# Kernel optimization log

Measured on AMD Instinct MI355X. Metric: run time of the kernel, lower is better.

The kernel has to match this reference:

```python
import jax, jax.numpy as jnp
import numpy as np

C = 512
C8 = C // 8  # 64
B, H, W = 4, 64, 64


def setup_inputs() -> dict:
    key = jax.random.key(0)
    ks = jax.random.split(key, 8)
    s_in = 1.0 / np.sqrt(C)
    return {
        "x": jax.random.normal(ks[0], (B, C, H, W), dtype=jnp.float32),
        "Wf": jax.random.normal(ks[1], (C8, C), dtype=jnp.float32) * s_in,
        "bf": jax.random.normal(ks[2], (C8,), dtype=jnp.float32) * 0.01,
        "Wg": jax.random.normal(ks[3], (C8, C), dtype=jnp.float32) * s_in,
        "bg": jax.random.normal(ks[4], (C8,), dtype=jnp.float32) * 0.01,
        "Wh": jax.random.normal(ks[5], (C, C), dtype=jnp.float32) * s_in,
        "bh": jax.random.normal(ks[6], (C,), dtype=jnp.float32) * 0.01,
        # original inits gamma=0; use small nonzero so the attention path is exercised
        "gamma": jax.random.normal(ks[7], (1,), dtype=jnp.float32) * 0.1,
    }


def reference(x, Wf, bf, Wg, bg, Wh, bh, gamma):
    b, c, h, w = x.shape
    n = h * w
    xt = x.reshape(b, c, n)  # flatten spatial -> tokens (b, C, N)
    # 1x1 convs are per-token GEMMs
    f = jnp.einsum('bcn,oc->bno', xt, Wf) + bf          # (b, N, C8)
    g = jnp.einsum('bcn,oc->bon', xt, Wg) + bg[:, None]  # (b, C8, N)
    attn = jax.nn.softmax(jnp.einsum('bnk,bkm->bnm', f, g), axis=2)  # (b, N, N)
    hv = jnp.einsum('bcn,oc->bon', xt, Wh) + bh[:, None]  # (b, C, N)
    # torch.bmm(h, attention): out[:,c,j] = sum_i h[:,c,i] * attn[:,i,j]
    sa = jnp.einsum('bci,bij->bcj', hv, attn).reshape(b, c, h, w)
    return gamma[0] * sa + x
```

## Files before the change

### kernel.cpp

```cpp
#include <hip/hip_runtime.h>


#define Bq 4
#define Cq 512
#define Nq 4096
#define PSTR 72

typedef __attribute__((ext_vector_type(8))) short bf16x8;
typedef __attribute__((ext_vector_type(4))) float f32x4;

__device__ __forceinline__ short f2bf(float f) {
  unsigned u = __float_as_uint(f);
  u += 0x7fffu + ((u >> 16) & 1u);
  return (short)(u >> 16);
}
__device__ __forceinline__ float bf2f(short h) {
  return __uint_as_float(((unsigned)(unsigned short)h) << 16);
}

#define MFMA16(A, B, C) __builtin_amdgcn_mfma_f32_16x16x32_bf16((A), (B), (C), 0, 0, 0)

__device__ __forceinline__ size_t fg_frag(int b, int t16, int ss) {
  return ((size_t)((b * 256 + t16) * 2 + ss)) * 512;
}
__device__ __forceinline__ size_t hv_frag(int b, int tc, int si) {
  return ((size_t)((b * 32 + tc) * 128 + si)) * 512;
}

__global__ __launch_bounds__(256) void k_prepw(
    const float* __restrict__ Wf, const float* __restrict__ Wg,
    const float* __restrict__ Wh,
    short* __restrict__ whi, short* __restrict__ wlo, short* __restrict__ whb) {
  int gid = blockIdx.x * 256 + threadIdx.x;
  if (gid < 128 * 512) {
    int row = gid >> 9;
    float v = (row < 64) ? Wf[gid] : Wg[gid - 32768];
    short h = f2bf(v);
    whi[gid] = h;
    wlo[gid] = f2bf(v - bf2f(h));
  }
  whb[gid] = f2bf(Wh[gid]);
}

__global__ __launch_bounds__(256) void k_xpose(
    const float* __restrict__ x, short* __restrict__ xthi, short* __restrict__ xtlo) {
  int b = blockIdx.z, c0 = blockIdx.y * 64, n0 = blockIdx.x * 64;
  __shared__ float tile[64][65];
  int t = threadIdx.x;
  int l = t & 15, g = t >> 4;
  const float* xp = x + ((size_t)b * Cq + c0) * Nq + n0;
#pragma unroll
  for (int e = 0; e < 4; e++) {
    int cl = g + e * 16;
    float4 v = *(const float4*)(xp + (size_t)cl * Nq + l * 4);
    tile[cl][l * 4 + 0] = v.x; tile[cl][l * 4 + 1] = v.y;
    tile[cl][l * 4 + 2] = v.z; tile[cl][l * 4 + 3] = v.w;
  }
  __syncthreads();
#pragma unroll
  for (int e = 0; e < 4; e++) {
    int nl = g + e * 16;
    short hi[4], lo[4];
#pragma unroll
    for (int qq = 0; qq < 4; qq++) {
      float v = tile[l * 4 + qq][nl];
      hi[qq] = f2bf(v);
      lo[qq] = f2bf(v - bf2f(hi[qq]));
    }
    size_t off = ((size_t)b * Nq + n0 + nl) * Cq + c0 + l * 4;
    *(short4*)(xthi + off) = make_short4(hi[0], hi[1], hi[2], hi[3]);
    *(short4*)(xtlo + off) = make_short4(lo[0], lo[1], lo[2], lo[3]);
  }
}

__global__ __launch_bounds__(512) void k_fg(
    const short* __restrict__ xthi, const short* __restrict__ xtlo,
    const short* __restrict__ whi, const short* __restrict__ wlo,
    const float* __restrict__ bfv, const float* __restrict__ bgv,
    short* __restrict__ ffh, short* __restrict__ ffl,
    short* __restrict__ gfh, short* __restrict__ gfl) {
  int b = blockIdx.y, n0 = blockIdx.x * 64;
  int t = threadIdx.x, w = t >> 6, lane = t & 63, l15 = lane & 15, q = lane >> 4;
  int wr = w & 3, wh = w >> 2;
  const short* ah = xthi + ((size_t)b * Nq + n0 + wr * 16 + l15) * Cq;
  const short* al = xtlo + ((size_t)b * Nq + n0 + wr * 16 + l15) * Cq;
  f32x4 z = {0.f, 0.f, 0.f, 0.f};
  f32x4 acc[4] = {z, z, z, z};
  for (int ks = 0; ks < 16; ks++) {
    bf16x8 Ahi = *(const bf16x8*)(ah + ks * 32 + q * 8);
    bf16x8 Alo = *(const bf16x8*)(al + ks * 32 + q * 8);
#pragma unroll
    for (int os = 0; os < 4; os++) {
      int o = wh * 64 + os * 16 + l15;
      bf16x8 Bhi = *(const bf16x8*)(whi + o * 512 + ks * 32 + q * 8);
      bf16x8 Blo = *(const bf16x8*)(wlo + o * 512 + ks * 32 + q * 8);
      acc[os] = MFMA16(Alo, Bhi, acc[os]);
      acc[os] = MFMA16(Ahi, Blo, acc[os]);
      acc[os] = MFMA16(Ahi, Bhi, acc[os]);
    }
  }
#pragma unroll
  for (int os = 0; os < 4; os++) {
#pragma unroll
    for (int r = 0; r < 4; r++) {
      int o = os * 16 + l15;
      int n = n0 + wr * 16 + q * 4 + r;
      float v = acc[os][r] + (wh == 0 ? bfv[o] : bgv[o]);
      size_t off = ((size_t)((b * 256 + (n >> 4)) * 2 + (o >> 5))) * 512
                 + (((o >> 3) & 3) * 16 + (n & 15)) * 8 + (o & 7);
      short h = f2bf(v);
      short lo = f2bf(v - bf2f(h));
      if (wh == 0) { ffh[off] = h; ffl[off] = lo; }
      else         { gfh[off] = h; gfl[off] = lo; }
    }
  }
}

__global__ __launch_bounds__(512) void k_stats(
    const short* __restrict__ ffh, const short* __restrict__ ffl,
    const short* __restrict__ gfh, const short* __restrict__ gfl,
    float* __restrict__ lsum4) {
  int jch = blockIdx.x, jc = jch * 1024, i0 = blockIdx.y * 64, b = blockIdx.z;
  int t = threadIdx.x, w = t >> 6, lane = t & 63, l15 = lane & 15, q = lane >> 4;
  bf16x8 Ahi[4][2], Alo[4][2];
#pragma unroll
  for (int ig = 0; ig < 4; ig++)
#pragma unroll
    for (int ss = 0; ss < 2; ss++) {
      size_t base = fg_frag(b, (i0 >> 4) + ig, ss) + lane * 8;
      Ahi[ig][ss] = *(const bf16x8*)(ffh + base);
      Alo[ig][ss] = *(const bf16x8*)(ffl + base);
    }
  float ls[16];
#pragma unroll
  for (int a = 0; a < 16; a++) ls[a] = 0.f;
  f32x4 z = {0.f, 0.f, 0.f, 0.f};
  for (int jt = 0; jt < 8; jt++) {
    int tj = (jc >> 4) + w * 8 + jt;
    bf16x8 GBh[2], GBl[2];
#pragma unroll
    for (int ss = 0; ss < 2; ss++) {
      size_t base = fg_frag(b, tj, ss) + lane * 8;
      GBh[ss] = *(const bf16x8*)(gfh + base);
      GBl[ss] = *(const bf16x8*)(gfl + base);
    }
#pragma unroll
    for (int ig = 0; ig < 4; ig++) {
      f32x4 sh = z, sl = z;
#pragma unroll
      for (int ss = 0; ss < 2; ss++) {
        sl = MFMA16(Alo[ig][ss], GBh[ss], sl);
        sl = MFMA16(Ahi[ig][ss], GBl[ss], sl);
        sh = MFMA16(Ahi[ig][ss], GBh[ss], sh);
      }
#pragma unroll
      for (int r = 0; r < 4; r++) ls[ig * 4 + r] += __expf(sh[r] + sl[r]);
    }
  }
#pragma unroll
  for (int m = 1; m < 16; m <<= 1) {
#pragma unroll
    for (int a = 0; a < 16; a++) ls[a] += __shfl_xor(ls[a], m, 64);
  }
  __shared__ float part[8][64];
  if (l15 == 0) {
#pragma unroll
    for (int ig = 0; ig < 4; ig++)
#pragma unroll
      for (int r = 0; r < 4; r++) part[w][ig * 16 + q * 4 + r] = ls[ig * 4 + r];
  }
  __syncthreads();
  if (t < 64) {
    float s = 0.f;
#pragma unroll
    for (int ww = 0; ww < 8; ww++) s += part[ww][t];
    lsum4[(size_t)jch * 16384 + (size_t)b * Nq + i0 + t] = s;
  }
}

__global__ __launch_bounds__(512) void k_hv(
    const short* __restrict__ whb, const short* __restrict__ xthi,
    const float* __restrict__ bhv, const float* __restrict__ lsum4,
    short* __restrict__ hvf) {
  int si = blockIdx.x, b = blockIdx.y;
  int t = threadIdx.x, w = t >> 6, lane = t & 63, l15 = lane & 15, q = lane >> 4;
  int c0 = w * 64;
  const short* ar0 = xthi + ((size_t)b * Nq + si * 32 + l15) * Cq;
  const short* ar1 = ar0 + 16 * Cq;
  f32x4 z = {0.f, 0.f, 0.f, 0.f};
  f32x4 acc[2][4];
#pragma unroll
  for (int a = 0; a < 2; a++)
#pragma unroll
    for (int c = 0; c < 4; c++) acc[a][c] = z;
  for (int ks = 0; ks < 16; ks++) {
    bf16x8 A0 = *(const bf16x8*)(ar0 + ks * 32 + q * 8);
    bf16x8 A1 = *(const bf16x8*)(ar1 + ks * 32 + q * 8);
#pragma unroll
    for (int ct = 0; ct < 4; ct++) {
      bf16x8 Bv = *(const bf16x8*)(whb + (size_t)(c0 + ct * 16 + l15) * 512 + ks * 32 + q * 8);
      acc[0][ct] = MFMA16(A0, Bv, acc[0][ct]);
      acc[1][ct] = MFMA16(A1, Bv, acc[1][ct]);
    }
  }
  float li[2][4];
#pragma unroll
  for (int it = 0; it < 2; it++)
#pragma unroll
    for (int r = 0; r < 4; r++) {
      size_t idx = (size_t)b * Nq + si * 32 + it * 16 + q * 4 + r;
      float s = lsum4[idx] + lsum4[16384 + idx] + lsum4[32768 + idx] + lsum4[49152 + idx];
      li[it][r] = 1.0f / s;
    }
  int src0 = ((q & 1) << 5) + l15;
  int src1 = src0 + 16;
  int hiSel = q >> 1;
#pragma unroll
  for (int ct = 0; ct < 4; ct++) {
    float bias = bhv[c0 + ct * 16 + l15];
    unsigned u01[2], u23[2];
#pragma unroll
    for (int it = 0; it < 2; it++) {
      float v0 = (acc[it][ct][0] + bias) * li[it][0];
      float v1 = (acc[it][ct][1] + bias) * li[it][1];
      float v2 = (acc[it][ct][2] + bias) * li[it][2];
      float v3 = (acc[it][ct][3] + bias) * li[it][3];
      u01[it] = (unsigned)(unsigned short)f2bf(v0) | ((unsigned)(unsigned short)f2bf(v1) << 16);
      u23[it] = (unsigned)(unsigned short)f2bf(v2) | ((unsigned)(unsigned short)f2bf(v3) << 16);
    }
    unsigned a0 = __shfl((int)u01[0], src0), b0 = __shfl((int)u01[1], src0);
    unsigned a1 = __shfl((int)u23[0], src0), b1 = __shfl((int)u23[1], src0);
    unsigned a2 = __shfl((int)u01[0], src1), b2 = __shfl((int)u01[1], src1);
    unsigned a3 = __shfl((int)u23[0], src1), b3 = __shfl((int)u23[1], src1);
    uint4 st;
    st.x = hiSel ? b0 : a0;
    st.y = hiSel ? b1 : a1;
    st.z = hiSel ? b2 : a2;
    st.w = hiSel ? b3 : a3;
    *(uint4*)(hvf + hv_frag(b, (c0 >> 4) + ct, si) + (size_t)lane * 8) = st;
  }
}

__global__ __launch_bounds__(512, 2) void k_attn(
    const short* __restrict__ ffh, const short* __restrict__ ffl,
    const short* __restrict__ gfh, const short* __restrict__ gfl,
    const short* __restrict__ hvf, const float* __restrict__ x,
    const float* __restrict__ gp, float* __restrict__ out) {
  int L = blockIdx.x;
  int b = (L & 7) >> 1;
  int jt64 = ((L >> 3) << 1) | (L & 1);
  int j0 = jt64 * 64;
  int t = threadIdx.x, w = t >> 6, lane = t & 63, l15 = lane & 15, q = lane >> 4;
  int iq = w & 3, jh = w >> 2;
  __shared__ __align__(16) short pt[2][64 * PSTR];
  float gamma = gp[0];
  f32x4 z = {0.f, 0.f, 0.f, 0.f};
  f32x4 acc[4][4];
#pragma unroll
  for (int a = 0; a < 4; a++)
#pragma unroll
    for (int bb = 0; bb < 4; bb++) acc[a][bb] = z;
  bf16x8 GBh[2][2], GBl[2][2];
#pragma unroll
  for (int jt = 0; jt < 2; jt++)
#pragma unroll
    for (int ss = 0; ss < 2; ss++) {
      size_t base = fg_frag(b, (j0 >> 4) + jh * 2 + jt, ss) + lane * 8;
      GBh[jt][ss] = *(const bf16x8*)(gfh + base);
      GBl[jt][ss] = *(const bf16x8*)(gfl + base);
    }

  auto computeS = [&](int it, int buf) {
    bf16x8 Ah[2], Al[2];
#pragma unroll
    for (int ss = 0; ss < 2; ss++) {
      size_t base = fg_frag(b, it * 4 + iq, ss) + lane * 8;
      Ah[ss] = *(const bf16x8*)(ffh + base);
      Al[ss] = *(const bf16x8*)(ffl + base);
    }
#pragma unroll
    for (int jt = 0; jt < 2; jt++) {
      f32x4 sh = z, sl = z;
#pragma unroll
      for (int ss = 0; ss < 2; ss++) {
        sl = MFMA16(Al[ss], GBh[jt][ss], sl);
        sl = MFMA16(Ah[ss], GBl[jt][ss], sl);
        sh = MFMA16(Ah[ss], GBh[jt][ss], sh);
      }
      unsigned p01 = (unsigned)(unsigned short)f2bf(__expf(sh[0] + sl[0])) |
                     ((unsigned)(unsigned short)f2bf(__expf(sh[1] + sl[1])) << 16);
      unsigned p23 = (unsigned)(unsigned short)f2bf(__expf(sh[2] + sl[2])) |
                     ((unsigned)(unsigned short)f2bf(__expf(sh[3] + sl[3])) << 16);
      uint2 pv; pv.x = p01; pv.y = p23;
      *(uint2*)(&pt[buf][(jh * 32 + jt * 16 + l15) * PSTR + iq * 16 + q * 4]) = pv;
    }
  };

  computeS(0, 0);
  for (int it = 0; it < 64; it++) {
    __syncthreads();
    int buf = it & 1;
    if (it < 63) computeS(it + 1, 1 - buf);
#pragma unroll
    for (int ss = 0; ss < 2; ss++) {
      bf16x8 PB[4];
#pragma unroll
      for (int jt = 0; jt < 4; jt++)
        PB[jt] = *(const bf16x8*)(&pt[buf][(jt * 16 + l15) * PSTR + ss * 32 + q * 8]);
#pragma unroll
      for (int ct = 0; ct < 4; ct++) {
        size_t hb = hv_frag(b, w * 4 + ct, it * 2 + ss) + lane * 8;
        bf16x8 A = *(const bf16x8*)(hvf + hb);
#pragma unroll
        for (int jt = 0; jt < 4; jt++)
          acc[ct][jt] = MFMA16(A, PB[jt], acc[ct][jt]);
      }
    }
  }
#pragma unroll
  for (int ct = 0; ct < 4; ct++) {
#pragma unroll
    for (int jt = 0; jt < 4; jt++) {
#pragma unroll
      for (int r = 0; r < 4; r++) {
        int c = w * 64 + ct * 16 + q * 4 + r;
        int j = j0 + jt * 16 + l15;
        size_t off = ((size_t)b * Cq + c) * Nq + j;
        out[off] = gamma * acc[ct][jt][r] + x[off];
      }
    }
  }
}

extern "C" void kernel_launch(void* const* d_in, const int* in_sizes, int n_in,
                              void* d_out, int out_size, void* d_ws, size_t ws_size,
                              hipStream_t stream) {
  (void)in_sizes; (void)n_in; (void)out_size; (void)ws_size;
  const float* x  = (const float*)d_in[0];
  const float* Wf = (const float*)d_in[1];
  const float* bf = (const float*)d_in[2];
  const float* Wg = (const float*)d_in[3];
  const float* bg = (const float*)d_in[4];
  const float* Wh = (const float*)d_in[5];
  const float* bh = (const float*)d_in[6];
  const float* gm = (const float*)d_in[7];
  float* out = (float*)d_out;
  char* ws = (char*)d_ws;
  short* xthi  = (short*)(ws);
  short* xtlo  = (short*)(ws + 16777216);
  short* ffh   = (short*)(ws + 33554432);
  short* ffl   = (short*)(ws + 35651584);
  short* gfh   = (short*)(ws + 37748736);
  short* gfl   = (short*)(ws + 39845888);
  short* whi   = (short*)(ws + 41943040);
  short* wlo   = (short*)(ws + 42074112);
  short* whb   = (short*)(ws + 42205184);
  float* lsum4 = (float*)(ws + 42729472);
  short* hvf   = (short*)(ws + 42991616);

  hipLaunchKernelGGL(k_prepw, dim3(1024), dim3(256), 0, stream, Wf, Wg, Wh, whi, wlo, whb);
  hipLaunchKernelGGL(k_xpose, dim3(64, 8, 4), dim3(256), 0, stream, x, xthi, xtlo);
  hipLaunchKernelGGL(k_fg, dim3(64, 4), dim3(512), 0, stream,
                     xthi, xtlo, whi, wlo, bf, bg, ffh, ffl, gfh, gfl);
  hipLaunchKernelGGL(k_stats, dim3(4, 64, 4), dim3(512), 0, stream, ffh, ffl, gfh, gfl, lsum4);
  hipLaunchKernelGGL(k_hv, dim3(128, 4), dim3(512), 0, stream, whb, xthi, bh, lsum4, hvf);
  hipLaunchKernelGGL(k_attn, dim3(256), dim3(512), 0, stream,
                     ffh, ffl, gfh, gfl, hvf, x, gm, out);
}
```

Baseline: 337.7 us.

## Double k_attn workgroup to 1024 threads, splitting S tile and PV columns

The attention kernel now launches 1024 threads (16 waves) per block instead of 512. Each wave computes one 16x16 S tile instead of two, and a 64x32 slice of the output accumulator instead of 64x64. Accumulator and G-fragment registers per wave are halved, which allows more waves in flight to hide global-load latency on the hv fragments and the exp work. In exchange each hv fragment is now loaded by two waves, doubling hv read traffic, and the launch bound of (1024,4) may force register spills or fail to be met.

```diff
diff --git a/kernel.cpp b/kernel.cpp
--- a/kernel.cpp
+++ b/kernel.cpp
@@ -241,7 +241,7 @@
   }
 }
 
-__global__ __launch_bounds__(512, 2) void k_attn(
+__global__ __launch_bounds__(1024, 4) void k_attn(
     const short* __restrict__ ffh, const short* __restrict__ ffl,
     const short* __restrict__ gfh, const short* __restrict__ gfl,
     const short* __restrict__ hvf, const float* __restrict__ x,
@@ -252,23 +252,22 @@
   int j0 = jt64 * 64;
   int t = threadIdx.x, w = t >> 6, lane = t & 63, l15 = lane & 15, q = lane >> 4;
   int iq = w & 3, jh = w >> 2;
+  int cg = w & 7, jg = w >> 3;
   __shared__ __align__(16) short pt[2][64 * PSTR];
   float gamma = gp[0];
   f32x4 z = {0.f, 0.f, 0.f, 0.f};
-  f32x4 acc[4][4];
+  f32x4 acc[4][2];
 #pragma unroll
   for (int a = 0; a < 4; a++)
 #pragma unroll
-    for (int bb = 0; bb < 4; bb++) acc[a][bb] = z;
-  bf16x8 GBh[2][2], GBl[2][2];
-#pragma unroll
-  for (int jt = 0; jt < 2; jt++)
-#pragma unroll
-    for (int ss = 0; ss < 2; ss++) {
-      size_t base = fg_frag(b, (j0 >> 4) + jh * 2 + jt, ss) + lane * 8;
-      GBh[jt][ss] = *(const bf16x8*)(gfh + base);
-      GBl[jt][ss] = *(const bf16x8*)(gfl + base);
-    }
+    for (int bb = 0; bb < 2; bb++) acc[a][bb] = z;
+  bf16x8 GBh[2], GBl[2];
+#pragma unroll
+  for (int ss = 0; ss < 2; ss++) {
+    size_t base = fg_frag(b, (j0 >> 4) + jh, ss) + lane * 8;
+    GBh[ss] = *(const bf16x8*)(gfh + base);
+    GBl[ss] = *(const bf16x8*)(gfl + base);
+  }
 
   auto computeS = [&](int it, int buf) {
     bf16x8 Ah[2], Al[2];
@@ -278,22 +277,19 @@
       Ah[ss] = *(const bf16x8*)(ffh + base);
       Al[ss] = *(const bf16x8*)(ffl + base);
     }
-#pragma unroll
-    for (int jt = 0; jt < 2; jt++) {
-      f32x4 sh = z, sl = z;
-#pragma unroll
-      for (int ss = 0; ss < 2; ss++) {
-        sl = MFMA16(Al[ss], GBh[jt][ss], sl);
-        sl = MFMA16(Ah[ss], GBl[jt][ss], sl);
-        sh = MFMA16(Ah[ss], GBh[jt][ss], sh);
-      }
-      unsigned p01 = (unsigned)(unsigned short)f2bf(__expf(sh[0] + sl[0])) |
-                     ((unsigned)(unsigned short)f2bf(__expf(sh[1] + sl[1])) << 16);
-      unsigned p23 = (unsigned)(unsigned short)f2bf(__expf(sh[2] + sl[2])) |
-                     ((unsigned)(unsigned short)f2bf(__expf(sh[3] + sl[3])) << 16);
-      uint2 pv; pv.x = p01; pv.y = p23;
-      *(uint2*)(&pt[buf][(jh * 32 + jt * 16 + l15) * PSTR + iq * 16 + q * 4]) = pv;
-    }
+    f32x4 sh = z, sl = z;
+#pragma unroll
+    for (int ss = 0; ss < 2; ss++) {
+      sl = MFMA16(Al[ss], GBh[ss], sl);
+      sl = MFMA16(Ah[ss], GBl[ss], sl);
+      sh = MFMA16(Ah[ss], GBh[ss], sh);
+    }
+    unsigned p01 = (unsigned)(unsigned short)f2bf(__expf(sh[0] + sl[0])) |
+                   ((unsigned)(unsigned short)f2bf(__expf(sh[1] + sl[1])) << 16);
+    unsigned p23 = (unsigned)(unsigned short)f2bf(__expf(sh[2] + sl[2])) |
+                   ((unsigned)(unsigned short)f2bf(__expf(sh[3] + sl[3])) << 16);
+    uint2 pv; pv.x = p01; pv.y = p23;
+    *(uint2*)(&pt[buf][(jh * 16 + l15) * PSTR + iq * 16 + q * 4]) = pv;
   };
 
   computeS(0, 0);
@@ -303,16 +299,16 @@
     if (it < 63) computeS(it + 1, 1 - buf);
 #pragma unroll
     for (int ss = 0; ss < 2; ss++) {
-      bf16x8 PB[4];
-#pragma unroll
-      for (int jt = 0; jt < 4; jt++)
-        PB[jt] = *(const bf16x8*)(&pt[buf][(jt * 16 + l15) * PSTR + ss * 32 + q * 8]);
+      bf16x8 PB[2];
+#pragma unroll
+      for (int jt = 0; jt < 2; jt++)
+        PB[jt] = *(const bf16x8*)(&pt[buf][(jg * 32 + jt * 16 + l15) * PSTR + ss * 32 + q * 8]);
 #pragma unroll
       for (int ct = 0; ct < 4; ct++) {
-        size_t hb = hv_frag(b, w * 4 + ct, it * 2 + ss) + lane * 8;
+        size_t hb = hv_frag(b, cg * 4 + ct, it * 2 + ss) + lane * 8;
         bf16x8 A = *(const bf16x8*)(hvf + hb);
 #pragma unroll
-        for (int jt = 0; jt < 4; jt++)
+        for (int jt = 0; jt < 2; jt++)
           acc[ct][jt] = MFMA16(A, PB[jt], acc[ct][jt]);
       }
     }
@@ -320,11 +316,11 @@
 #pragma unroll
   for (int ct = 0; ct < 4; ct++) {
 #pragma unroll
-    for (int jt = 0; jt < 4; jt++) {
+    for (int jt = 0; jt < 2; jt++) {
 #pragma unroll
       for (int r = 0; r < 4; r++) {
-        int c = w * 64 + ct * 16 + q * 4 + r;
-        int j = j0 + jt * 16 + l15;
+        int c = cg * 64 + ct * 16 + q * 4 + r;
+        int j = j0 + jg * 32 + jt * 16 + l15;
         size_t off = ((size_t)b * Cq + c) * Nq + j;
         out[off] = gamma * acc[ct][jt][r] + x[off];
       }
@@ -364,6 +360,6 @@
                      xthi, xtlo, whi, wlo, bf, bg, ffh, ffl, gfh, gfl);
   hipLaunchKernelGGL(k_stats, dim3(4, 64, 4), dim3(512), 0, stream, ffh, ffl, gfh, gfl, lsum4);
   hipLaunchKernelGGL(k_hv, dim3(128, 4), dim3(512), 0, stream, whb, xthi, bh, lsum4, hvf);
-  hipLaunchKernelGGL(k_attn, dim3(256), dim3(512), 0, stream,
+  hipLaunchKernelGGL(k_attn, dim3(256), dim3(1024), 0, stream,
                      ffh, ffl, gfh, gfl, hvf, x, gm, out);
 }
```

Result: slower. 359.7 us (+6.5%).

## Retile attention kernel to 128-column j tiles split over channel halves

Applied to the files above, without the earlier changes.

Each block now covers 128 output columns and half of the 512 channels, where before it covered 64 columns and all channels. Each wave holds 2x8 accumulator tiles instead of 4x4. The aim is to reuse each loaded hv fragment across more P columns and cut hv global traffic per FLOP. The cost is that the exp-score computation (S = f·g) is done twice, once per channel half, and the shared P buffer doubles in size.

```diff
diff --git a/kernel.cpp b/kernel.cpp
--- a/kernel.cpp
+++ b/kernel.cpp
@@ -247,52 +247,56 @@
     const short* __restrict__ hvf, const float* __restrict__ x,
     const float* __restrict__ gp, float* __restrict__ out) {
   int L = blockIdx.x;
-  int b = (L & 7) >> 1;
-  int jt64 = ((L >> 3) << 1) | (L & 1);
-  int j0 = jt64 * 64;
+  int combo = L & 7;
+  int b = combo >> 1, ch = combo & 1;
+  int j0 = (L >> 3) << 7;
   int t = threadIdx.x, w = t >> 6, lane = t & 63, l15 = lane & 15, q = lane >> 4;
-  int iq = w & 3, jh = w >> 2;
-  __shared__ __align__(16) short pt[2][64 * PSTR];
+  int iq2 = w & 1, jq = w >> 1;
+  __shared__ __align__(16) short pt[2][128 * PSTR];
   float gamma = gp[0];
   f32x4 z = {0.f, 0.f, 0.f, 0.f};
-  f32x4 acc[4][4];
-#pragma unroll
-  for (int a = 0; a < 4; a++)
-#pragma unroll
-    for (int bb = 0; bb < 4; bb++) acc[a][bb] = z;
+  f32x4 acc[2][8];
+#pragma unroll
+  for (int a = 0; a < 2; a++)
+#pragma unroll
+    for (int bb = 0; bb < 8; bb++) acc[a][bb] = z;
   bf16x8 GBh[2][2], GBl[2][2];
 #pragma unroll
   for (int jt = 0; jt < 2; jt++)
 #pragma unroll
     for (int ss = 0; ss < 2; ss++) {
-      size_t base = fg_frag(b, (j0 >> 4) + jh * 2 + jt, ss) + lane * 8;
+      size_t base = fg_frag(b, (j0 >> 4) + jq * 2 + jt, ss) + lane * 8;
       GBh[jt][ss] = *(const bf16x8*)(gfh + base);
       GBl[jt][ss] = *(const bf16x8*)(gfl + base);
     }
 
   auto computeS = [&](int it, int buf) {
-    bf16x8 Ah[2], Al[2];
-#pragma unroll
-    for (int ss = 0; ss < 2; ss++) {
-      size_t base = fg_frag(b, it * 4 + iq, ss) + lane * 8;
-      Ah[ss] = *(const bf16x8*)(ffh + base);
-      Al[ss] = *(const bf16x8*)(ffl + base);
-    }
-#pragma unroll
-    for (int jt = 0; jt < 2; jt++) {
-      f32x4 sh = z, sl = z;
+#pragma unroll
+    for (int itl = 0; itl < 2; itl++) {
+      bf16x8 Ah[2], Al[2];
 #pragma unroll
       for (int ss = 0; ss < 2; ss++) {
-        sl = MFMA16(Al[ss], GBh[jt][ss], sl);
-        sl = MFMA16(Ah[ss], GBl[jt][ss], sl);
-        sh = MFMA16(Ah[ss], GBh[jt][ss], sh);
-      }
-      unsigned p01 = (unsigned)(unsigned short)f2bf(__expf(sh[0] + sl[0])) |
-                     ((unsigned)(unsigned short)f2bf(__expf(sh[1] + sl[1])) << 16);
-      unsigned p23 = (unsigned)(unsigned short)f2bf(__expf(sh[2] + sl[2])) |
-                     ((unsigned)(unsigned short)f2bf(__expf(sh[3] + sl[3])) << 16);
-      uint2 pv; pv.x = p01; pv.y = p23;
-      *(uint2*)(&pt[buf][(jh * 32 + jt * 16 + l15) * PSTR + iq * 16 + q * 4]) = pv;
+        size_t base = fg_frag(b, it * 4 + iq2 * 2 + itl, ss) + lane * 8;
+        Ah[ss] = *(const bf16x8*)(ffh + base);
+        Al[ss] = *(const bf16x8*)(ffl + base);
+      }
+#pragma unroll
+      for (int jt = 0; jt < 2; jt++) {
+        f32x4 sh = z, sl = z;
+#pragma unroll
+        for (int ss = 0; ss < 2; ss++) {
+          sl = MFMA16(Al[ss], GBh[jt][ss], sl);
+          sl = MFMA16(Ah[ss], GBl[jt][ss], sl);
+          sh = MFMA16(Ah[ss], GBh[jt][ss], sh);
+        }
+        unsigned p01 = (unsigned)(unsigned short)f2bf(__expf(sh[0] + sl[0])) |
+                       ((unsigned)(unsigned short)f2bf(__expf(sh[1] + sl[1])) << 16);
+        unsigned p23 = (unsigned)(unsigned short)f2bf(__expf(sh[2] + sl[2])) |
+                       ((unsigned)(unsigned short)f2bf(__expf(sh[3] + sl[3])) << 16);
+        uint2 pv; pv.x = p01; pv.y = p23;
+        *(uint2*)(&pt[buf][(jq * 32 + jt * 16 + l15) * PSTR +
+                           iq2 * 32 + itl * 16 + q * 4]) = pv;
+      }
     }
   };
 
@@ -303,30 +307,30 @@
     if (it < 63) computeS(it + 1, 1 - buf);
 #pragma unroll
     for (int ss = 0; ss < 2; ss++) {
-      bf16x8 PB[4];
-#pragma unroll
-      for (int jt = 0; jt < 4; jt++)
+      bf16x8 PB[8];
+#pragma unroll
+      for (int jt = 0; jt < 8; jt++)
         PB[jt] = *(const bf16x8*)(&pt[buf][(jt * 16 + l15) * PSTR + ss * 32 + q * 8]);
 #pragma unroll
-      for (int ct = 0; ct < 4; ct++) {
-        size_t hb = hv_frag(b, w * 4 + ct, it * 2 + ss) + lane * 8;
+      for (int ctl = 0; ctl < 2; ctl++) {
+        size_t hb = hv_frag(b, ch * 16 + w * 2 + ctl, it * 2 + ss) + lane * 8;
         bf16x8 A = *(const bf16x8*)(hvf + hb);
 #pragma unroll
-        for (int jt = 0; jt < 4; jt++)
-          acc[ct][jt] = MFMA16(A, PB[jt], acc[ct][jt]);
-      }
-    }
-  }
-#pragma unroll
-  for (int ct = 0; ct < 4; ct++) {
-#pragma unroll
-    for (int jt = 0; jt < 4; jt++) {
+        for (int jt = 0; jt < 8; jt++)
+          acc[ctl][jt] = MFMA16(A, PB[jt], acc[ctl][jt]);
+      }
+    }
+  }
+#pragma unroll
+  for (int ctl = 0; ctl < 2; ctl++) {
+#pragma unroll
+    for (int jt = 0; jt < 8; jt++) {
 #pragma unroll
       for (int r = 0; r < 4; r++) {
-        int c = w * 64 + ct * 16 + q * 4 + r;
+        int c = ch * 256 + w * 32 + ctl * 16 + q * 4 + r;
         int j = j0 + jt * 16 + l15;
         size_t off = ((size_t)b * Cq + c) * Nq + j;
-        out[off] = gamma * acc[ct][jt][r] + x[off];
+        out[off] = gamma * acc[ctl][jt][r] + x[off];
       }
     }
   }
```

Measured after the change: 400.7 us. 18.6% more time.
